# Performance work log

Measured on AMD Instinct MI355X. Metric: run time of the kernel, lower is better.

The kernel has to match this reference:

```python
import jax, jax.numpy as jnp
import numpy as np

B, N, D, F = 4096, 64, 64, 4096
KP_DIM = N * (N + 1) // 2  # 2080
# static row-major triu/tril index lists (matches torch.masked_select ordering)
_TRIU_I, _TRIU_J = (np.array(a) for a in np.triu_indices(N, 0))
_TRIL_I, _TRIL_J = (np.array(a) for a in np.tril_indices(N, 0))


def setup_inputs() -> dict:
    key = jax.random.key(0)
    k1, k2, k3, k4 = jax.random.split(key, 4)
    feature_emb = jax.random.normal(k1, (B, N, D), dtype=jnp.float32)
    # xavier_normal for [D, D]
    std = float(np.sqrt(2.0 / (D + D)))
    kp_W = jax.random.normal(k2, (D, D), dtype=jnp.float32) * std
    # nn.Linear weights are [out_features, in_features]
    bound = float(1.0 / np.sqrt(KP_DIM))
    W_triu = jax.random.uniform(k3, (F, KP_DIM), dtype=jnp.float32, minval=-bound, maxval=bound)
    W_tril = jax.random.uniform(k4, (F, KP_DIM), dtype=jnp.float32, minval=-bound, maxval=bound)
    return {"feature_emb": feature_emb, "kp_W": kp_W, "W_triu": W_triu, "W_tril": W_tril}


def reference(feature_emb, kp_W, W_triu, W_tril):
    # embs_kp[b,i,j] = e[b,i,:] @ kp_W @ e[b,j,:]  -> [B, N, N]
    embs_kp = jnp.einsum("bnd,de,bme->bnm", feature_emb, kp_W, feature_emb)
    triu = embs_kp[:, _TRIU_I, _TRIU_J]  # [B, kp_dim], row-major order
    tril = embs_kp[:, _TRIL_I, _TRIL_J]  # [B, kp_dim]
    embs_flatten = feature_emb.reshape(feature_emb.shape[0], -1)  # [B, N*D]
    view_1 = triu @ W_triu.T  # [B, F]
    view_2 = tril @ W_tril.T  # [B, F]
    return (embs_flatten, view_1, view_2)
```

## Files before the change

### kernel.cpp

```cpp
#include <hip/hip_runtime.h>

typedef __bf16 bf16x8 __attribute__((ext_vector_type(8)));
typedef float f32x4 __attribute__((ext_vector_type(4)));
typedef unsigned short u16x4 __attribute__((ext_vector_type(4)));
typedef unsigned short u16x8 __attribute__((ext_vector_type(8)));

#define KP 2112
#define NT 33

__device__ __forceinline__ unsigned short f2bf(float f) {
  unsigned int u = __builtin_bit_cast(unsigned int, f);
  u += 0x7FFFu + ((u >> 16) & 1u);
  return (unsigned short)(u >> 16);
}

__device__ __forceinline__ bf16x8 ld_frag(const unsigned short* p) {
  return __builtin_bit_cast(bf16x8, *(const u16x8*)p);
}

#define MFMA16(a, b, c) __builtin_amdgcn_mfma_f32_16x16x32_bf16((a), (b), (c), 0, 0, 0)

__device__ __forceinline__ void cp16(const void* g, void* l) {
  __builtin_amdgcn_global_load_lds(
      (const __attribute__((address_space(1))) unsigned int*)g,
      (__attribute__((address_space(3))) unsigned int*)l, 16, 0, 0);
}

__device__ __forceinline__ void gate() {
  __builtin_amdgcn_s_barrier();
  asm volatile("s_waitcnt lgkmcnt(0)" ::: "memory");
  __builtin_amdgcn_sched_barrier(0);
}
__device__ __forceinline__ void close_bar() {
  asm volatile("" ::: "memory");
  __builtin_amdgcn_s_barrier();
  __builtin_amdgcn_sched_barrier(0);
}

#define VMWAIT(N) asm volatile("s_waitcnt vmcnt(" #N ")" ::: "memory")

__device__ __forceinline__ void emit_tri(const unsigned short* __restrict__ sK,
                                         unsigned short* __restrict__ dst,
                                         bool upper, int tid) {
#pragma unroll
  for (int jj = 0; jj < 2; ++jj) {
    if (jj == 1 && tid >= 8) break;
    const int p0 = (jj == 0) ? tid * 8 : 2048 + tid * 8;
    int i, j;
    if (upper) {
      float s = sqrtf(4160.25f - 2.0f * (float)p0);
      i = (int)(64.5f - s);
      if (i < 0) i = 0;
      if (i > 63) i = 63;
      while (i > 0 && i * (129 - i) / 2 > p0) --i;
      while (i < 63 && (i + 1) * (128 - i) / 2 <= p0) ++i;
      j = i + (p0 - i * (129 - i) / 2);
    } else {
      float s = sqrtf(8.0f * (float)p0 + 1.0f);
      i = (int)((s - 1.0f) * 0.5f);
      if (i < 0) i = 0;
      if (i > 63) i = 63;
      while (i > 0 && i * (i + 1) / 2 > p0) --i;
      while (i < 63 && (i + 1) * (i + 2) / 2 <= p0) ++i;
      j = p0 - i * (i + 1) / 2;
    }
    u16x8 o;
#pragma unroll
    for (int e = 0; e < 8; ++e) {
      const int p = p0 + e;
      o[e] = (p < 2080 && i < 64) ? sK[i * 64 + j] : (unsigned short)0;
      if (upper) { if (++j > 63) { ++i; j = i; } }
      else       { if (++j > i)  { ++i; j = 0; } }
    }
    *(u16x8*)(dst + p0) = o;
  }
}

__global__ __launch_bounds__(256) void prep_all(
    const float* __restrict__ E,
    const float* __restrict__ Wkp,
    const float* __restrict__ Wtriu,
    const float* __restrict__ Wtril,
    float* __restrict__ out0,
    unsigned short* __restrict__ triu,
    unsigned short* __restrict__ tril,
    unsigned short* __restrict__ Wu,
    unsigned short* __restrict__ Wl)
{
  const int bid = blockIdx.x;
  const int tid = threadIdx.x;

  if (bid >= 4096) {
    const int r0 = (bid - 4096) * 2;
#pragma unroll
    for (int q = 0; q < 4; ++q) {
      const int row = r0 + (q & 1);
      const float* src = (q < 2 ? Wtriu : Wtril) + (size_t)row * 2080;
      unsigned short* dst = (q < 2 ? Wu : Wl) + (size_t)row * KP;
      for (int c = tid; c < 528; c += 256) {
        u16x4 o = {0, 0, 0, 0};
        if (c < 520) {
          float4 v = *(const float4*)(src + c * 4);
          o[0] = f2bf(v.x); o[1] = f2bf(v.y); o[2] = f2bf(v.z); o[3] = f2bf(v.w);
        }
        ((u16x4*)dst)[c] = o;
      }
    }
    return;
  }

  __shared__ __align__(16) unsigned short sE[64 * 64];
  __shared__ __align__(16) unsigned short sWt[64 * 64];
  __shared__ __align__(16) unsigned short sT[64 * 64];

  const int b = bid;
  const float* Eb = E + (size_t)b * 4096;
  float* o0 = out0 + (size_t)b * 4096;

#pragma unroll
  for (int it = 0; it < 4; ++it) {
    const int flat = it * 1024 + tid * 4;
    float4 v = *(const float4*)(Eb + flat);
    *(float4*)(o0 + flat) = v;
    u16x4 e;
    e[0] = f2bf(v.x); e[1] = f2bf(v.y); e[2] = f2bf(v.z); e[3] = f2bf(v.w);
    *(u16x4*)(sE + flat) = e;
    float4 wv = *(const float4*)(Wkp + flat);
    const int d = flat >> 6, c0 = flat & 63;
    sWt[(c0 + 0) * 64 + d] = f2bf(wv.x);
    sWt[(c0 + 1) * 64 + d] = f2bf(wv.y);
    sWt[(c0 + 2) * 64 + d] = f2bf(wv.z);
    sWt[(c0 + 3) * 64 + d] = f2bf(wv.w);
  }
  __syncthreads();

  const int lane = tid & 63, w = tid >> 6;
  const int fr = lane & 15;
  const int fk = (lane >> 4) << 3;
  const int qr = (lane >> 4) << 2;

#pragma unroll
  for (int ct = 0; ct < 4; ++ct) {
    f32x4 acc = {0.f, 0.f, 0.f, 0.f};
#pragma unroll
    for (int k2 = 0; k2 < 2; ++k2) {
      bf16x8 a = ld_frag(sE + (w * 16 + fr) * 64 + k2 * 32 + fk);
      bf16x8 bb = ld_frag(sWt + (ct * 16 + fr) * 64 + k2 * 32 + fk);
      acc = MFMA16(a, bb, acc);
    }
#pragma unroll
    for (int r = 0; r < 4; ++r)
      sT[(w * 16 + qr + r) * 64 + ct * 16 + fr] = f2bf(acc[r]);
  }
  __syncthreads();

  unsigned short* sK = sWt;
#pragma unroll
  for (int ct = 0; ct < 4; ++ct) {
    f32x4 acc = {0.f, 0.f, 0.f, 0.f};
#pragma unroll
    for (int k2 = 0; k2 < 2; ++k2) {
      bf16x8 a = ld_frag(sT + (w * 16 + fr) * 64 + k2 * 32 + fk);
      bf16x8 bb = ld_frag(sE + (ct * 16 + fr) * 64 + k2 * 32 + fk);
      acc = MFMA16(a, bb, acc);
    }
#pragma unroll
    for (int r = 0; r < 4; ++r)
      sK[(w * 16 + qr + r) * 64 + ct * 16 + fr] = f2bf(acc[r]);
  }
  __syncthreads();

  emit_tri(sK, triu + (size_t)b * KP, true, tid);
  emit_tri(sK, tril + (size_t)b * KP, false, tid);
}

__global__ __launch_bounds__(512, 2) void gemm_views(
    const unsigned short* __restrict__ triu, const unsigned short* __restrict__ tril,
    const unsigned short* __restrict__ Wu, const unsigned short* __restrict__ Wl,
    float* __restrict__ dout)
{
  __shared__ __align__(16) unsigned short lds[65536];

  const int z = blockIdx.z;
  const unsigned short* Ag = z ? tril : triu;
  const unsigned short* Bg = z ? Wl : Wu;
  float* C = dout + (size_t)16777216 * (size_t)(1 + z);

  const int tid = threadIdx.x;
  const int lane = tid & 63, wv = tid >> 6;
  const int m0 = blockIdx.y << 8, n0 = blockIdx.x << 8;

  const int lr = lane >> 3;
  const int cuch = (lane & 7) ^ lr;
  const int rA = wv * 8 + lr;
  const int rB = (wv & 3) * 8 + (wv >> 2) * 64 + lr;
  const unsigned short* gA = Ag + (size_t)(m0 + rA) * KP + cuch * 8;
  const unsigned short* gB = Bg + (size_t)(n0 + rB) * KP + cuch * 8;
  const int dA = tid * 8;
  const int dB = (wv & 3) * 512 + (wv >> 2) * 4096 + lane * 8;

  const int fr = lane & 15, fq = lane >> 4;
  const int rowA0 = (wv >> 2) * 128 + fr;
  const int rowB0 = (wv & 3) * 64 + fr;

  f32x4 acc[8][4] = {};
  bf16x8 a_[4], aX_[4], b0_[4], b1_[4];

#define STAGE_A(B_, KT, OFF) do { \
    cp16(gA + (size_t)(OFF) * KP + (KT) * 64, lds + (B_) * 32768 + (OFF) * 64 + dA); \
    cp16(gA + (size_t)((OFF) + 128) * KP + (KT) * 64, \
         lds + (B_) * 32768 + ((OFF) + 128) * 64 + dA); \
  } while (0)
#define STAGE_B(B_, KT, OFF) do { \
    cp16(gB + (size_t)(OFF) * KP + (KT) * 64, \
         lds + (B_) * 32768 + 16384 + (OFF) * 64 + dB); \
    cp16(gB + (size_t)((OFF) + 128) * KP + (KT) * 64, \
         lds + (B_) * 32768 + 16384 + ((OFF) + 128) * 64 + dB); \
  } while (0)
#define LDA(S, B_, MH, KH) do { _Pragma("unroll") \
    for (int mt = 0; mt < 4; ++mt) \
      S[mt] = ld_frag(lds + (B_) * 32768 + (rowA0 + (MH) * 64 + mt * 16) * 64 + \
                      ((((KH) * 4 + fq) ^ (fr & 7)) * 8)); \
  } while (0)
#define LDB(S, B_, KH) do { _Pragma("unroll") \
    for (int nt = 0; nt < 4; ++nt) \
      S[nt] = ld_frag(lds + (B_) * 32768 + 16384 + (rowB0 + nt * 16) * 64 + \
                      ((((KH) * 4 + fq) ^ (fr & 7)) * 8)); \
  } while (0)
#define PH_MFMA(AS, BS, MH) do { \
    __builtin_amdgcn_s_setprio(1); \
    _Pragma("unroll") for (int mt = 0; mt < 4; ++mt) \
    _Pragma("unroll") for (int nt = 0; nt < 4; ++nt) \
      acc[(MH) * 4 + mt][nt] = MFMA16(AS[mt], BS[nt], acc[(MH) * 4 + mt][nt]); \
    __builtin_amdgcn_s_setprio(0); \
  } while (0)

  STAGE_A(0, 0, 0);
  STAGE_B(0, 0, 0);
  STAGE_B(0, 0, 32);
  STAGE_A(0, 0, 64);
  STAGE_B(1, 1, 0);
  STAGE_B(1, 1, 32);
  STAGE_A(1, 1, 0);
  VMWAIT(6);
  close_bar();

  for (int t = 0; t < NT; ++t) {
    const int cb = t & 1, nb = cb ^ 1;
    const int t1 = (t + 1 < NT) ? t + 1 : NT - 1;
    const int t2 = (t + 2 < NT) ? t + 2 : NT - 1;
    LDA(a_, cb, 0, 0);
    LDB(b0_, cb, 0);
    STAGE_A(nb, t1, 64);
    gate();
    PH_MFMA(a_, b0_, 0);
    close_bar();
    LDA(a_, cb, 1, 0);
    LDB(b1_, cb, 1);
    gate();
    PH_MFMA(a_, b0_, 1);
    close_bar();
    LDA(a_, cb, 1, 1);
    LDA(aX_, cb, 0, 1);
    STAGE_B(cb, t2, 0);
    gate();
    PH_MFMA(a_, b1_, 1);
    VMWAIT(4);
    close_bar();
    STAGE_B(cb, t2, 32);
    STAGE_A(cb, t2, 0);
    gate();
    PH_MFMA(aX_, b1_, 0);
    VMWAIT(6);
    close_bar();
  }

  const int qr = fq << 2;
  const int crow = m0 + (wv >> 2) * 128 + qr;
  const int ccol = n0 + (wv & 3) * 64 + fr;
#pragma unroll
  for (int mt = 0; mt < 8; ++mt)
#pragma unroll
    for (int nt = 0; nt < 4; ++nt) {
      float* cp = C + (size_t)(crow + mt * 16) * 4096 + (ccol + nt * 16);
#pragma unroll
      for (int r = 0; r < 4; ++r) cp[(size_t)r * 4096] = acc[mt][nt][r];
    }
#undef STAGE_A
#undef STAGE_B
#undef LDA
#undef LDB
#undef PH_MFMA
}

extern "C" void kernel_launch(void* const* d_in, const int* in_sizes, int n_in,
                              void* d_out, int out_size, void* d_ws, size_t ws_size,
                              hipStream_t stream) {
  const float* feat  = (const float*)d_in[0];
  const float* kpW   = (const float*)d_in[1];
  const float* Wtriu = (const float*)d_in[2];
  const float* Wtril = (const float*)d_in[3];
  float* out = (float*)d_out;

  const size_t per = (size_t)4096 * KP;
  unsigned short* triu_bf = (unsigned short*)d_ws;
  unsigned short* tril_bf = triu_bf + per;
  unsigned short* Wu_bf   = tril_bf + per;
  unsigned short* Wl_bf   = Wu_bf + per;

  prep_all<<<dim3(6144), dim3(256), 0, stream>>>(
      feat, kpW, Wtriu, Wtril, out, triu_bf, tril_bf, Wu_bf, Wl_bf);
  gemm_views<<<dim3(16, 16, 2), dim3(512), 0, stream>>>(triu_bf, tril_bf, Wu_bf, Wl_bf, out);
}
```

Baseline: 424.0 us.

## Replace 4-phase pipelined GEMM with simple 16-wave double-buffered K=32 loop

The view GEMM moves from 512 threads, each wave holding a 128x64 accumulator tile with a hand-scheduled four-phase pipeline over K=64 stages, to 1024 threads with 64x64 per wave. It now uses a plain double-buffered loop over K=32 tiles with one barrier per step. This cuts LDS to 64 KB and registers per wave, trading fewer MFMAs per fragment load and more barrier iterations for more waves to hide latency. The new loop waits on vmcnt(0) every step, so load latency is exposed more often.

```diff
diff --git a/kernel.cpp b/kernel.cpp
--- a/kernel.cpp
+++ b/kernel.cpp
@@ -6,7 +6,7 @@
 typedef unsigned short u16x8 __attribute__((ext_vector_type(8)));
 
 #define KP 2112
-#define NT 33
+#define NKT 66
 
 __device__ __forceinline__ unsigned short f2bf(float f) {
   unsigned int u = __builtin_bit_cast(unsigned int, f);
@@ -26,11 +26,6 @@
       (__attribute__((address_space(3))) unsigned int*)l, 16, 0, 0);
 }
 
-__device__ __forceinline__ void gate() {
-  __builtin_amdgcn_s_barrier();
-  asm volatile("s_waitcnt lgkmcnt(0)" ::: "memory");
-  __builtin_amdgcn_sched_barrier(0);
-}
 __device__ __forceinline__ void close_bar() {
   asm volatile("" ::: "memory");
   __builtin_amdgcn_s_barrier();
@@ -174,12 +169,12 @@
   emit_tri(sK, tril + (size_t)b * KP, false, tid);
 }
 
-__global__ __launch_bounds__(512, 2) void gemm_views(
+__global__ __launch_bounds__(1024, 2) void gemm_views(
     const unsigned short* __restrict__ triu, const unsigned short* __restrict__ tril,
     const unsigned short* __restrict__ Wu, const unsigned short* __restrict__ Wl,
     float* __restrict__ dout)
 {
-  __shared__ __align__(16) unsigned short lds[65536];
+  __shared__ __align__(16) unsigned short lds[32768];
 
   const int z = blockIdx.z;
   const unsigned short* Ag = z ? tril : triu;
@@ -190,107 +185,59 @@
   const int lane = tid & 63, wv = tid >> 6;
   const int m0 = blockIdx.y << 8, n0 = blockIdx.x << 8;
 
-  const int lr = lane >> 3;
-  const int cuch = (lane & 7) ^ lr;
-  const int rA = wv * 8 + lr;
-  const int rB = (wv & 3) * 8 + (wv >> 2) * 64 + lr;
-  const unsigned short* gA = Ag + (size_t)(m0 + rA) * KP + cuch * 8;
-  const unsigned short* gB = Bg + (size_t)(n0 + rB) * KP + cuch * 8;
-  const int dA = tid * 8;
-  const int dB = (wv & 3) * 512 + (wv >> 2) * 4096 + lane * 8;
+  const int srow = tid >> 2;
+  const int schk = (tid & 3) ^ (srow & 3);
+  const unsigned short* gA = Ag + (size_t)(m0 + srow) * KP + schk * 8;
+  const unsigned short* gB = Bg + (size_t)(n0 + srow) * KP + schk * 8;
+  unsigned short* const dstA = lds + tid * 8;
+  unsigned short* const dstB = lds + 8192 + tid * 8;
 
   const int fr = lane & 15, fq = lane >> 4;
-  const int rowA0 = (wv >> 2) * 128 + fr;
-  const int rowB0 = (wv & 3) * 64 + fr;
-
-  f32x4 acc[8][4] = {};
-  bf16x8 a_[4], aX_[4], b0_[4], b1_[4];
-
-#define STAGE_A(B_, KT, OFF) do { \
-    cp16(gA + (size_t)(OFF) * KP + (KT) * 64, lds + (B_) * 32768 + (OFF) * 64 + dA); \
-    cp16(gA + (size_t)((OFF) + 128) * KP + (KT) * 64, \
-         lds + (B_) * 32768 + ((OFF) + 128) * 64 + dA); \
-  } while (0)
-#define STAGE_B(B_, KT, OFF) do { \
-    cp16(gB + (size_t)(OFF) * KP + (KT) * 64, \
-         lds + (B_) * 32768 + 16384 + (OFF) * 64 + dB); \
-    cp16(gB + (size_t)((OFF) + 128) * KP + (KT) * 64, \
-         lds + (B_) * 32768 + 16384 + ((OFF) + 128) * 64 + dB); \
-  } while (0)
-#define LDA(S, B_, MH, KH) do { _Pragma("unroll") \
-    for (int mt = 0; mt < 4; ++mt) \
-      S[mt] = ld_frag(lds + (B_) * 32768 + (rowA0 + (MH) * 64 + mt * 16) * 64 + \
-                      ((((KH) * 4 + fq) ^ (fr & 7)) * 8)); \
-  } while (0)
-#define LDB(S, B_, KH) do { _Pragma("unroll") \
-    for (int nt = 0; nt < 4; ++nt) \
-      S[nt] = ld_frag(lds + (B_) * 32768 + 16384 + (rowB0 + nt * 16) * 64 + \
-                      ((((KH) * 4 + fq) ^ (fr & 7)) * 8)); \
-  } while (0)
-#define PH_MFMA(AS, BS, MH) do { \
-    __builtin_amdgcn_s_setprio(1); \
-    _Pragma("unroll") for (int mt = 0; mt < 4; ++mt) \
-    _Pragma("unroll") for (int nt = 0; nt < 4; ++nt) \
-      acc[(MH) * 4 + mt][nt] = MFMA16(AS[mt], BS[nt], acc[(MH) * 4 + mt][nt]); \
-    __builtin_amdgcn_s_setprio(0); \
-  } while (0)
-
-  STAGE_A(0, 0, 0);
-  STAGE_B(0, 0, 0);
-  STAGE_B(0, 0, 32);
-  STAGE_A(0, 0, 64);
-  STAGE_B(1, 1, 0);
-  STAGE_B(1, 1, 32);
-  STAGE_A(1, 1, 0);
-  VMWAIT(6);
+  const int wm = (wv >> 2) << 6, wn = (wv & 3) << 6;
+  const int kx = (fq ^ (fr & 3)) * 8;
+
+  f32x4 acc[4][4] = {};
+  bf16x8 a_[4], b_[4];
+
+  cp16(gA, dstA);
+  cp16(gB, dstB);
+  VMWAIT(0);
   close_bar();
 
-  for (int t = 0; t < NT; ++t) {
+  for (int t = 0; t < NKT; ++t) {
     const int cb = t & 1, nb = cb ^ 1;
-    const int t1 = (t + 1 < NT) ? t + 1 : NT - 1;
-    const int t2 = (t + 2 < NT) ? t + 2 : NT - 1;
-    LDA(a_, cb, 0, 0);
-    LDB(b0_, cb, 0);
-    STAGE_A(nb, t1, 64);
-    gate();
-    PH_MFMA(a_, b0_, 0);
+    const int tn = (t + 1 < NKT) ? t + 1 : NKT - 1;
+    cp16(gA + tn * 32, dstA + nb * 16384);
+    cp16(gB + tn * 32, dstB + nb * 16384);
+    const unsigned short* ba = lds + cb * 16384;
+#pragma unroll
+    for (int mt = 0; mt < 4; ++mt)
+      a_[mt] = ld_frag(ba + (wm + mt * 16 + fr) * 32 + kx);
+#pragma unroll
+    for (int nt = 0; nt < 4; ++nt)
+      b_[nt] = ld_frag(ba + 8192 + (wn + nt * 16 + fr) * 32 + kx);
+    __builtin_amdgcn_s_setprio(1);
+#pragma unroll
+    for (int mt = 0; mt < 4; ++mt)
+#pragma unroll
+      for (int nt = 0; nt < 4; ++nt)
+        acc[mt][nt] = MFMA16(a_[mt], b_[nt], acc[mt][nt]);
+    __builtin_amdgcn_s_setprio(0);
+    VMWAIT(0);
     close_bar();
-    LDA(a_, cb, 1, 0);
-    LDB(b1_, cb, 1);
-    gate();
-    PH_MFMA(a_, b0_, 1);
-    close_bar();
-    LDA(a_, cb, 1, 1);
-    LDA(aX_, cb, 0, 1);
-    STAGE_B(cb, t2, 0);
-    gate();
-    PH_MFMA(a_, b1_, 1);
-    VMWAIT(4);
-    close_bar();
-    STAGE_B(cb, t2, 32);
-    STAGE_A(cb, t2, 0);
-    gate();
-    PH_MFMA(aX_, b1_, 0);
-    VMWAIT(6);
-    close_bar();
   }
 
   const int qr = fq << 2;
-  const int crow = m0 + (wv >> 2) * 128 + qr;
-  const int ccol = n0 + (wv & 3) * 64 + fr;
-#pragma unroll
-  for (int mt = 0; mt < 8; ++mt)
+  const int crow = m0 + wm + qr;
+  const int ccol = n0 + wn + fr;
+#pragma unroll
+  for (int mt = 0; mt < 4; ++mt)
 #pragma unroll
     for (int nt = 0; nt < 4; ++nt) {
       float* cp = C + (size_t)(crow + mt * 16) * 4096 + (ccol + nt * 16);
 #pragma unroll
       for (int r = 0; r < 4; ++r) cp[(size_t)r * 4096] = acc[mt][nt][r];
     }
-#undef STAGE_A
-#undef STAGE_B
-#undef LDA
-#undef LDB
-#undef PH_MFMA
 }
 
 extern "C" void kernel_launch(void* const* d_in, const int* in_sizes, int n_in,
@@ -310,5 +257,5 @@
 
   prep_all<<<dim3(6144), dim3(256), 0, stream>>>(
       feat, kpW, Wtriu, Wtril, out, triu_bf, tril_bf, Wu_bf, Wl_bf);
-  gemm_views<<<dim3(16, 16, 2), dim3(512), 0, stream>>>(triu_bf, tril_bf, Wu_bf, Wl_bf, out);
-}
+  gemm_views<<<dim3(16, 16, 2), dim3(1024), 0, stream>>>(triu_bf, tril_bf, Wu_bf, Wl_bf, out);
+}
```

Measured after the change: 440.9 us. +4.0%, slower.
